# Kernel tuning notes

Measured on AMD Instinct MI355X. Metric: run time of the kernel, lower is better.

## Reference

```python
import jax, jax.numpy as jnp
import numpy as np
import math

B, SQ, SK, H, NH = 8, 512, 512, 768, 12
DH = H // NH

def setup_inputs() -> dict:
    key = jax.random.key(0)
    ks = jax.random.split(key, 8)
    s = 1.0 / math.sqrt(H)
    return {
        "hidden_states": jax.random.normal(ks[0], (B, SQ, H), jnp.float32),
        "context": jax.random.normal(ks[1], (B, SK, H), jnp.float32),
        "attention_mask": jax.random.randint(ks[2], (B, SK), 0, 2, jnp.int32),
        "Wq": jax.random.normal(ks[3], (H, H), jnp.float32) * s,
        "bq": jnp.zeros((H,), jnp.float32),
        "Wk": jax.random.normal(ks[4], (H, H), jnp.float32) * s,
        "bk": jnp.zeros((H,), jnp.float32),
        "Wv": jax.random.normal(ks[5], (H, H), jnp.float32) * s,
        "bv": jnp.zeros((H,), jnp.float32),
        "abs_pos_emb": jax.random.normal(ks[6], (512, DH), jnp.float32),
    }

def _heads(x):
    # [B, S, H] -> [B, NH, S, DH]
    b, s, _ = x.shape
    return x.reshape(b, s, NH, DH).transpose(0, 2, 1, 3)

def reference(hidden_states, context, attention_mask, Wq, bq, Wk, bk, Wv, bv, abs_pos_emb):
    q = _heads(hidden_states @ Wq.T + bq)   # [B,NH,SQ,DH]
    k = _heads(context @ Wk.T + bk)         # [B,NH,SK,DH]
    v = _heads(context @ Wv.T + bv)         # [B,NH,SK,DH]
    scores = jnp.einsum('bhqd,bhkd->bhqk', q, k)
    pos_k = abs_pos_emb[:context.shape[1]]          # [SK, DH]
    pos_q = abs_pos_emb[:hidden_states.shape[1]]    # [SQ, DH]
    pos_scores = jnp.einsum('bhqd,kd->bhqk', q + pos_q[None, None], pos_k)
    scores = (scores + pos_scores) / jnp.sqrt(jnp.float32(DH))
    mask_bias = jnp.where(attention_mask[:, None, None, :] == 0,
                          -jnp.inf, 0.0).astype(scores.dtype)
    scores = scores + mask_bias
    probs = jax.nn.softmax(scores, axis=-1)  # dropout is identity in eval
    out = jnp.einsum('bhqk,bhkd->bhqd', probs, v)
    b, _, sq, _ = out.shape
    return out.transpose(0, 2, 1, 3).reshape(b, sq, NH * DH)
```

## Files before the change

kernel.cpp:

```cpp
#include <hip/hip_runtime.h>
#include <stdint.h>

#define B_   8
#define SQ_  512
#define SK_  512
#define H_   768
#define NH_  12
#define DH_  64
#define BH_  (B_*NH_)
#define M_   (B_*SQ_)
#define NTOT (3*H_)

typedef __attribute__((ext_vector_type(8))) short short8;
typedef __attribute__((ext_vector_type(4))) float floatx4;
typedef __attribute__((ext_vector_type(4))) unsigned int uint4v;
typedef __attribute__((ext_vector_type(4))) unsigned short ushort4v;

#define MFMA16(a, b, c) __builtin_amdgcn_mfma_f32_16x16x32_bf16((a), (b), (c), 0, 0, 0)

__device__ __forceinline__ unsigned short f2b(float f) {
  union { float f; unsigned u; } c; c.f = f;
  unsigned r = (c.u + 0x7fffu + ((c.u >> 16) & 1u)) >> 16;
  return (unsigned short)r;
}
__device__ __forceinline__ float b2f(unsigned short u) {
  union { float f; unsigned u; } c; c.u = ((unsigned)u) << 16;
  return c.f;
}
__device__ __forceinline__ short8 ld8(const unsigned short* p) {
  union { uint4v u; short8 s; } c;
  c.u = *(const uint4v*)p;
  return c.s;
}

#define SEG_X   (M_*H_)
#define SEG_XC  (2*SEG_X)
#define SEG_W1  (H_*H_)
#define SEG_WE  (SEG_XC + 3*SEG_W1)
#define SEG_BE  (SEG_WE + NTOT)
#define SEG_PE  (SEG_BE + SQ_*DH_)

__global__ __launch_bounds__(256) void pack_kernel(
    const float* __restrict__ hid, const float* __restrict__ ctx,
    const float* __restrict__ Wq, const float* __restrict__ Wk, const float* __restrict__ Wv,
    const float* __restrict__ bq, const float* __restrict__ bk, const float* __restrict__ bv,
    const float* __restrict__ pos,
    unsigned short* __restrict__ Xh, unsigned short* __restrict__ Xc,
    unsigned short* __restrict__ Wa, float* __restrict__ Ba,
    unsigned short* __restrict__ Pb)
{
  int i = (blockIdx.x * 256 + threadIdx.x) * 4;
  if (i < SEG_X) {
    floatx4 v = *(const floatx4*)(hid + i);
    ushort4v o = { f2b(v.x), f2b(v.y), f2b(v.z), f2b(v.w) };
    *(ushort4v*)(Xh + i) = o;
  } else if (i < SEG_XC) {
    int j = i - SEG_X;
    floatx4 v = *(const floatx4*)(ctx + j);
    ushort4v o = { f2b(v.x), f2b(v.y), f2b(v.z), f2b(v.w) };
    *(ushort4v*)(Xc + j) = o;
  } else if (i < SEG_WE) {
    int j = i - SEG_XC;
    const float* src; int o;
    if (j < SEG_W1)        { src = Wq; o = j; }
    else if (j < 2*SEG_W1) { src = Wk; o = j - SEG_W1; }
    else                   { src = Wv; o = j - 2*SEG_W1; }
    floatx4 v = *(const floatx4*)(src + o);
    ushort4v ov = { f2b(v.x), f2b(v.y), f2b(v.z), f2b(v.w) };
    *(ushort4v*)(Wa + j) = ov;
  } else if (i < SEG_BE) {
    int j = i - SEG_WE;
    #pragma unroll
    for (int t = 0; t < 4; ++t) {
      int jj = j + t;
      float v = (jj < H_) ? bq[jj] : (jj < 2*H_) ? bk[jj - H_] : bv[jj - 2*H_];
      Ba[jj] = v;
    }
  } else if (i < SEG_PE) {
    int j = i - SEG_BE;
    floatx4 v = *(const floatx4*)(pos + j);
    ushort4v o = { f2b(v.x), f2b(v.y), f2b(v.z), f2b(v.w) };
    *(ushort4v*)(Pb + j) = o;
  }
}

__global__ __launch_bounds__(256) void qkv_gemm(
    const unsigned short* __restrict__ Xh, const unsigned short* __restrict__ Xc,
    const unsigned short* __restrict__ W,  const float* __restrict__ bias,
    const unsigned short* __restrict__ Pb,
    unsigned short* __restrict__ qw, unsigned short* __restrict__ kw,
    unsigned short* __restrict__ vt)
{
  __shared__ unsigned short As[128][72];
  __shared__ unsigned short Bs[128][72];

  int bx = blockIdx.x;
  int xcd = bx & 7, j = bx >> 3;
  int bm = (xcd >> 1) * 8 + j / 9;
  int bn = (xcd & 1) * 9 + j % 9;
  const unsigned short* X = (bn < 6) ? Xh : Xc;
  bool isV = (bn >= 12);
  int m0 = bm * 128, n0 = bn * 128;

  int tid = threadIdx.x;
  int lane = tid & 63, wave = tid >> 6;
  int wm = (wave & 1) * 64, wn = (wave >> 1) * 64;
  int lc16 = lane & 15, quad = lane >> 4, kk = quad * 8;
  int srow = tid >> 3, sch = (tid & 7) * 8;

  unsigned short (*TA)[72] = isV ? As : Bs;
  unsigned short (*TB)[72] = isV ? Bs : As;
  int oa = isV ? wm : wn;
  int ob = isV ? wn : wm;

  floatx4 acc[4][4];
  #pragma unroll
  for (int i = 0; i < 4; ++i)
    #pragma unroll
    for (int jj = 0; jj < 4; ++jj) acc[i][jj] = (floatx4){0.f, 0.f, 0.f, 0.f};

  uint4v a[4], b[4];
  #pragma unroll
  for (int rp = 0; rp < 4; ++rp) {
    a[rp] = *(const uint4v*)&X[(m0 + srow + rp * 32) * H_ + sch];
    b[rp] = *(const uint4v*)&W[(n0 + srow + rp * 32) * H_ + sch];
  }

  for (int k0 = 0; k0 < H_; k0 += 64) {
    __syncthreads();
    #pragma unroll
    for (int rp = 0; rp < 4; ++rp) {
      *(uint4v*)&As[srow + rp * 32][sch] = a[rp];
      *(uint4v*)&Bs[srow + rp * 32][sch] = b[rp];
    }
    __syncthreads();

    if (k0 + 64 < H_) {
      #pragma unroll
      for (int rp = 0; rp < 4; ++rp) {
        a[rp] = *(const uint4v*)&X[(m0 + srow + rp * 32) * H_ + k0 + 64 + sch];
        b[rp] = *(const uint4v*)&W[(n0 + srow + rp * 32) * H_ + k0 + 64 + sch];
      }
    }

    #pragma unroll
    for (int s = 0; s < 2; ++s) {
      short8 af[4], bf[4];
      #pragma unroll
      for (int i = 0; i < 4; ++i) af[i] = ld8(&TA[oa + i * 16 + lc16][s * 32 + kk]);
      #pragma unroll
      for (int i = 0; i < 4; ++i) bf[i] = ld8(&TB[ob + i * 16 + lc16][s * 32 + kk]);
      #pragma unroll
      for (int mi = 0; mi < 4; ++mi)
        #pragma unroll
        for (int ni = 0; ni < 4; ++ni)
          acc[mi][ni] = MFMA16(af[mi], bf[ni], acc[mi][ni]);
    }
  }

  if (!isV) {
    #pragma unroll
    for (int mi = 0; mi < 4; ++mi) {
      #pragma unroll
      for (int ni = 0; ni < 4; ++ni) {
        int gn0 = n0 + wn + mi * 16 + quad * 4;
        int gs  = m0 + wm + ni * 16 + lc16;
        int bidx = gs >> 9, s0 = gs & 511;
        floatx4 bv4 = *(const floatx4*)&bias[gn0];
        ushort4v o;
        if (gn0 < H_) {
          int h = gn0 >> 6, d0 = gn0 & 63;
          #pragma unroll
          for (int r = 0; r < 4; ++r) o[r] = f2b(acc[mi][ni][r] + bv4[r]);
          *(ushort4v*)(qw + (((bidx * NH_ + h) << 9) + s0) * DH_ + d0) = o;
        } else {
          int g = gn0 - H_;
          int h = g >> 6, d0 = g & 63;
          ushort4v pk = *(const ushort4v*)(Pb + s0 * DH_ + d0);
          #pragma unroll
          for (int r = 0; r < 4; ++r) o[r] = f2b(acc[mi][ni][r] + bv4[r] + b2f(pk[r]));
          *(ushort4v*)(kw + (((bidx * NH_ + h) << 9) + s0) * DH_ + d0) = o;
        }
      }
    }
  } else {
    #pragma unroll
    for (int mi = 0; mi < 4; ++mi) {
      #pragma unroll
      for (int ni = 0; ni < 4; ++ni) {
        int gm0 = m0 + wm + mi * 16 + quad * 4;
        int gn  = n0 + wn + ni * 16 + lc16;
        float bv = bias[gn];
        int bidx = gm0 >> 9, s0 = gm0 & 511;
        int g = gn - 2 * H_;
        int h = g >> 6, d = g & 63;
        ushort4v pk;
        #pragma unroll
        for (int r = 0; r < 4; ++r) pk[r] = f2b(acc[mi][ni][r] + bv);
        *(ushort4v*)(vt + ((bidx * NH_ + h) * DH_ + d) * SK_ + s0) = pk;
      }
    }
  }
}

#define SCALE2 0.18033688011112042f
#define CPAD 136

__global__ __launch_bounds__(256) void attn_kernel(
    const unsigned short* __restrict__ qw, const unsigned short* __restrict__ kw,
    const unsigned short* __restrict__ vt, const unsigned short* __restrict__ posb,
    const int* __restrict__ mask, float* __restrict__ out)
{
  __shared__ unsigned short Sc[2][64][CPAD];
  __shared__ float mb2[SK_];
  __shared__ float red[64][4];

  int bx = blockIdx.x;
  int bh = bx % 96, qt = bx / 96;
  int b = bh / NH_, h = bh - b * NH_;
  int tid = threadIdx.x, lane = tid & 63, wave = tid >> 6;
  int lc16 = lane & 15, quad = lane >> 4, kk = quad * 8;

  for (int i = tid; i < SK_; i += 256)
    mb2[i] = mask[(b << 9) + i] ? 0.0f : -100000.0f;

  const unsigned short* qbase = qw + ((bh << 9) + qt * 64) * DH_;
  const unsigned short* pqb   = posb + (qt * 64) * DH_;
  short8 aq[4][2], ap[4][2];
  #pragma unroll
  for (int rt = 0; rt < 4; ++rt) {
    const unsigned short* qr = qbase + (rt * 16 + lc16) * DH_;
    const unsigned short* pr = pqb + (rt * 16 + lc16) * DH_;
    aq[rt][0] = ld8(qr + kk);
    aq[rt][1] = ld8(qr + 32 + kk);
    ap[rt][0] = ld8(pr + kk);
    ap[rt][1] = ld8(pr + 32 + kk);
  }

  const unsigned short* kwb = kw + ((bh << 9)) * DH_;
  const unsigned short* vb0 = vt + (bh * DH_ + wave * 16 + lc16) * SK_;
  float rs[4] = {0.f, 0.f, 0.f, 0.f};
  floatx4 o[4];
  #pragma unroll
  for (int i = 0; i < 4; ++i) o[i] = (floatx4){0.f, 0.f, 0.f, 0.f};

  short8 cb0, cb1, cp0, cp1, nb0, nb1, np0, np1;
  {
    int kcol = wave * 32;
    const unsigned short* kb = kwb + kcol * DH_;
    const unsigned short* pb = posb + kcol * DH_;
    cb0 = ld8(kb + lc16 * DH_ + kk);
    cb1 = ld8(kb + lc16 * DH_ + 32 + kk);
    cp0 = ld8(pb + lc16 * DH_ + kk);
    cp1 = ld8(pb + lc16 * DH_ + 32 + kk);
  }

  __syncthreads();

  for (int chunk = 0; chunk < 4; ++chunk) {
    unsigned short (*S)[CPAD] = Sc[chunk & 1];

    short8 vf[4];
    #pragma unroll
    for (int ks = 0; ks < 4; ++ks) vf[ks] = ld8(vb0 + chunk * 128 + ks * 32 + kk);

    #pragma unroll
    for (int ct = 0; ct < 2; ++ct) {
      int s = chunk * 2 + ct;
      if (s < 7) {
        int kcol = ((s + 1) >> 1) * 128 + wave * 32 + ((s + 1) & 1) * 16;
        const unsigned short* kb = kwb + kcol * DH_;
        const unsigned short* pb = posb + kcol * DH_;
        nb0 = ld8(kb + lc16 * DH_ + kk);
        nb1 = ld8(kb + lc16 * DH_ + 32 + kk);
        np0 = ld8(pb + lc16 * DH_ + kk);
        np1 = ld8(pb + lc16 * DH_ + 32 + kk);
      }
      int kcol = chunk * 128 + wave * 32 + ct * 16;
      floatx4 mk = *(const floatx4*)&mb2[kcol + quad * 4];
      floatx4 c[4];
      #pragma unroll
      for (int rt = 0; rt < 4; ++rt) {
        c[rt] = (floatx4){0.f, 0.f, 0.f, 0.f};
        c[rt] = MFMA16(cb0, aq[rt][0], c[rt]);
        c[rt] = MFMA16(cb1, aq[rt][1], c[rt]);
        c[rt] = MFMA16(cp0, ap[rt][0], c[rt]);
        c[rt] = MFMA16(cp1, ap[rt][1], c[rt]);
      }
      int lcol = wave * 32 + ct * 16 + quad * 4;
      #pragma unroll
      for (int rt = 0; rt < 4; ++rt) {
        ushort4v pv;
        float sum = 0.f;
        #pragma unroll
        for (int r = 0; r < 4; ++r) {
          float e = __builtin_exp2f(c[rt][r] * SCALE2 + mk[r]);
          sum += e;
          pv[r] = f2b(e);
        }
        rs[rt] += sum;
        *(ushort4v*)&S[rt * 16 + lc16][lcol] = pv;
      }
      cb0 = nb0; cb1 = nb1; cp0 = np0; cp1 = np1;
    }
    __syncthreads();

    #pragma unroll
    for (int ks = 0; ks < 4; ++ks) {
      #pragma unroll
      for (int rt = 0; rt < 4; ++rt) {
        short8 pa = ld8(&S[rt * 16 + lc16][ks * 32 + kk]);
        o[rt] = MFMA16(pa, vf[ks], o[rt]);
      }
    }
  }

  #pragma unroll
  for (int rt = 0; rt < 4; ++rt) {
    rs[rt] += __shfl_xor(rs[rt], 16, 64);
    rs[rt] += __shfl_xor(rs[rt], 32, 64);
  }
  if (quad == 0) {
    #pragma unroll
    for (int rt = 0; rt < 4; ++rt) red[rt * 16 + lc16][wave] = rs[rt];
  }
  __syncthreads();

  #pragma unroll
  for (int rt = 0; rt < 4; ++rt) {
    #pragma unroll
    for (int r = 0; r < 4; ++r) {
      int sl = rt * 16 + quad * 4 + r;
      float inv = 1.0f / (red[sl][0] + red[sl][1] + red[sl][2] + red[sl][3]);
      int s = qt * 64 + sl;
      out[((b << 9) + s) * H_ + h * DH_ + wave * 16 + lc16] = o[rt][r] * inv;
    }
  }
}

extern "C" void kernel_launch(void* const* d_in, const int* in_sizes, int n_in,
                              void* d_out, int out_size, void* d_ws, size_t ws_size,
                              hipStream_t stream) {
  (void)in_sizes; (void)n_in; (void)out_size; (void)ws_size;
  const float* hid  = (const float*)d_in[0];
  const float* ctx  = (const float*)d_in[1];
  const int*   mask = (const int*)d_in[2];
  const float* Wq   = (const float*)d_in[3];
  const float* bq   = (const float*)d_in[4];
  const float* Wk   = (const float*)d_in[5];
  const float* bk   = (const float*)d_in[6];
  const float* Wv   = (const float*)d_in[7];
  const float* bv   = (const float*)d_in[8];
  const float* pos  = (const float*)d_in[9];

  char* ws = (char*)d_ws;
  size_t off = 0;
  auto alloc = [&](size_t bytes) { char* p = ws + off; off = (off + bytes + 255) & ~(size_t)255; return p; };
  unsigned short* Xh = (unsigned short*)alloc((size_t)SEG_X * 2);
  unsigned short* Xc = (unsigned short*)alloc((size_t)SEG_X * 2);
  unsigned short* Wa = (unsigned short*)alloc((size_t)3 * SEG_W1 * 2);
  float*          Ba = (float*)alloc((size_t)NTOT * 4);
  unsigned short* qw = (unsigned short*)alloc((size_t)BH_ * SQ_ * DH_ * 2);
  unsigned short* kw = (unsigned short*)alloc((size_t)BH_ * SK_ * DH_ * 2);
  unsigned short* vt = (unsigned short*)alloc((size_t)BH_ * DH_ * SK_ * 2);
  unsigned short* Pb = (unsigned short*)alloc((size_t)SQ_ * DH_ * 2);

  int pack_blocks = (SEG_PE / 4 + 255) / 256;
  pack_kernel<<<pack_blocks, 256, 0, stream>>>(hid, ctx, Wq, Wk, Wv, bq, bk, bv, pos, Xh, Xc, Wa, Ba, Pb);
  qkv_gemm<<<32 * 18, 256, 0, stream>>>(Xh, Xc, Wa, Ba, Pb, qw, kw, vt);
  attn_kernel<<<BH_ * 8, 256, 0, stream>>>(qw, kw, vt, Pb, mask, (float*)d_out);
}
```

Measured before the change: 155.4 us.

## Fuse pack, QKV GEMM and attention into one persistent kernel with grid barriers

Merges the three kernel launches into a single 768-block kernel that uses atomic-counter grid barriers between the pack, GEMM and attention phases, with shared memory unioned across phases. This removes launch overhead and the inter-kernel gaps. In exchange it depends on all 768 blocks being co-resident (launch bounds of 3 blocks per CU), leaves 192 blocks idle during the GEMM phase, and adds spin-barrier cost plus a memset launch. If the blocks cannot all be resident at once, the barrier can deadlock.

```diff
diff --git a/kernel.cpp b/kernel.cpp
--- a/kernel.cpp
+++ b/kernel.cpp
@@ -10,6 +10,7 @@
 #define BH_  (B_*NH_)
 #define M_   (B_*SQ_)
 #define NTOT (3*H_)
+#define GRID_ 768
 
 typedef __attribute__((ext_vector_type(8))) short short8;
 typedef __attribute__((ext_vector_type(4))) float floatx4;
@@ -31,6 +32,18 @@
   union { uint4v u; short8 s; } c;
   c.u = *(const uint4v*)p;
   return c.s;
+}
+
+__device__ __forceinline__ void gsync(unsigned* c) {
+  __syncthreads();
+  if (threadIdx.x == 0) {
+    __threadfence();
+    __hip_atomic_fetch_add(c, 1u, __ATOMIC_RELEASE, __HIP_MEMORY_SCOPE_AGENT);
+    while (__hip_atomic_load(c, __ATOMIC_ACQUIRE, __HIP_MEMORY_SCOPE_AGENT) < GRID_)
+      __builtin_amdgcn_s_sleep(2);
+  }
+  __syncthreads();
+  __threadfence();
 }
 
 #define SEG_X   (M_*H_)
@@ -40,300 +53,303 @@
 #define SEG_BE  (SEG_WE + NTOT)
 #define SEG_PE  (SEG_BE + SQ_*DH_)
 
-__global__ __launch_bounds__(256) void pack_kernel(
+#define SCALE2 0.18033688011112042f
+#define CPAD 136
+
+struct __align__(16) SMemG { unsigned short As[128][72]; unsigned short Bs[128][72]; };
+struct __align__(16) SMemA {
+  unsigned short Sc[2][64][CPAD];
+  float mb2[SK_];
+  float red[64][4];
+};
+union SMemU { SMemG g; SMemA a; };
+
+__global__ __launch_bounds__(256, 3) void mega_kernel(
     const float* __restrict__ hid, const float* __restrict__ ctx,
-    const float* __restrict__ Wq, const float* __restrict__ Wk, const float* __restrict__ Wv,
-    const float* __restrict__ bq, const float* __restrict__ bk, const float* __restrict__ bv,
+    const int* __restrict__ mask,
+    const float* __restrict__ Wq, const float* __restrict__ bq,
+    const float* __restrict__ Wk, const float* __restrict__ bk,
+    const float* __restrict__ Wv, const float* __restrict__ bv,
     const float* __restrict__ pos,
     unsigned short* __restrict__ Xh, unsigned short* __restrict__ Xc,
     unsigned short* __restrict__ Wa, float* __restrict__ Ba,
-    unsigned short* __restrict__ Pb)
+    unsigned short* __restrict__ Pb,
+    unsigned short* __restrict__ qw, unsigned short* __restrict__ kw,
+    unsigned short* __restrict__ vt,
+    unsigned* __restrict__ bar, float* __restrict__ out)
 {
-  int i = (blockIdx.x * 256 + threadIdx.x) * 4;
-  if (i < SEG_X) {
-    floatx4 v = *(const floatx4*)(hid + i);
-    ushort4v o = { f2b(v.x), f2b(v.y), f2b(v.z), f2b(v.w) };
-    *(ushort4v*)(Xh + i) = o;
-  } else if (i < SEG_XC) {
-    int j = i - SEG_X;
-    floatx4 v = *(const floatx4*)(ctx + j);
-    ushort4v o = { f2b(v.x), f2b(v.y), f2b(v.z), f2b(v.w) };
-    *(ushort4v*)(Xc + j) = o;
-  } else if (i < SEG_WE) {
-    int j = i - SEG_XC;
-    const float* src; int o;
-    if (j < SEG_W1)        { src = Wq; o = j; }
-    else if (j < 2*SEG_W1) { src = Wk; o = j - SEG_W1; }
-    else                   { src = Wv; o = j - 2*SEG_W1; }
-    floatx4 v = *(const floatx4*)(src + o);
-    ushort4v ov = { f2b(v.x), f2b(v.y), f2b(v.z), f2b(v.w) };
-    *(ushort4v*)(Wa + j) = ov;
-  } else if (i < SEG_BE) {
-    int j = i - SEG_WE;
-    #pragma unroll
-    for (int t = 0; t < 4; ++t) {
-      int jj = j + t;
-      float v = (jj < H_) ? bq[jj] : (jj < 2*H_) ? bk[jj - H_] : bv[jj - 2*H_];
-      Ba[jj] = v;
-    }
-  } else if (i < SEG_PE) {
-    int j = i - SEG_BE;
-    floatx4 v = *(const floatx4*)(pos + j);
-    ushort4v o = { f2b(v.x), f2b(v.y), f2b(v.z), f2b(v.w) };
-    *(ushort4v*)(Pb + j) = o;
+  __shared__ SMemU sm;
+  const int bx = blockIdx.x;
+  const int tid = threadIdx.x;
+
+  for (int v = bx * 256 + tid; v < SEG_PE / 4; v += GRID_ * 256) {
+    int i = v * 4;
+    if (i < SEG_X) {
+      floatx4 val = *(const floatx4*)(hid + i);
+      ushort4v o = { f2b(val.x), f2b(val.y), f2b(val.z), f2b(val.w) };
+      *(ushort4v*)(Xh + i) = o;
+    } else if (i < SEG_XC) {
+      int j = i - SEG_X;
+      floatx4 val = *(const floatx4*)(ctx + j);
+      ushort4v o = { f2b(val.x), f2b(val.y), f2b(val.z), f2b(val.w) };
+      *(ushort4v*)(Xc + j) = o;
+    } else if (i < SEG_WE) {
+      int j = i - SEG_XC;
+      const float* src; int o;
+      if (j < SEG_W1)        { src = Wq; o = j; }
+      else if (j < 2*SEG_W1) { src = Wk; o = j - SEG_W1; }
+      else                   { src = Wv; o = j - 2*SEG_W1; }
+      floatx4 val = *(const floatx4*)(src + o);
+      ushort4v ov = { f2b(val.x), f2b(val.y), f2b(val.z), f2b(val.w) };
+      *(ushort4v*)(Wa + j) = ov;
+    } else if (i < SEG_BE) {
+      int j = i - SEG_WE;
+      #pragma unroll
+      for (int t = 0; t < 4; ++t) {
+        int jj = j + t;
+        float val = (jj < H_) ? bq[jj] : (jj < 2*H_) ? bk[jj - H_] : bv[jj - 2*H_];
+        Ba[jj] = val;
+      }
+    } else {
+      int j = i - SEG_BE;
+      floatx4 val = *(const floatx4*)(pos + j);
+      ushort4v o = { f2b(val.x), f2b(val.y), f2b(val.z), f2b(val.w) };
+      *(ushort4v*)(Pb + j) = o;
+    }
   }
-}
-
-__global__ __launch_bounds__(256) void qkv_gemm(
-    const unsigned short* __restrict__ Xh, const unsigned short* __restrict__ Xc,
-    const unsigned short* __restrict__ W,  const float* __restrict__ bias,
-    const unsigned short* __restrict__ Pb,
-    unsigned short* __restrict__ qw, unsigned short* __restrict__ kw,
-    unsigned short* __restrict__ vt)
-{
-  __shared__ unsigned short As[128][72];
-  __shared__ unsigned short Bs[128][72];
-
-  int bx = blockIdx.x;
-  int xcd = bx & 7, j = bx >> 3;
-  int bm = (xcd >> 1) * 8 + j / 9;
-  int bn = (xcd & 1) * 9 + j % 9;
-  const unsigned short* X = (bn < 6) ? Xh : Xc;
-  bool isV = (bn >= 12);
-  int m0 = bm * 128, n0 = bn * 128;
-
-  int tid = threadIdx.x;
-  int lane = tid & 63, wave = tid >> 6;
-  int wm = (wave & 1) * 64, wn = (wave >> 1) * 64;
-  int lc16 = lane & 15, quad = lane >> 4, kk = quad * 8;
-  int srow = tid >> 3, sch = (tid & 7) * 8;
-
-  unsigned short (*TA)[72] = isV ? As : Bs;
-  unsigned short (*TB)[72] = isV ? Bs : As;
-  int oa = isV ? wm : wn;
-  int ob = isV ? wn : wm;
-
-  floatx4 acc[4][4];
-  #pragma unroll
-  for (int i = 0; i < 4; ++i)
-    #pragma unroll
-    for (int jj = 0; jj < 4; ++jj) acc[i][jj] = (floatx4){0.f, 0.f, 0.f, 0.f};
-
-  uint4v a[4], b[4];
-  #pragma unroll
-  for (int rp = 0; rp < 4; ++rp) {
-    a[rp] = *(const uint4v*)&X[(m0 + srow + rp * 32) * H_ + sch];
-    b[rp] = *(const uint4v*)&W[(n0 + srow + rp * 32) * H_ + sch];
+
+  gsync(bar + 0);
+
+  if (bx < 576) {
+    int xcd = bx & 7, j = bx >> 3;
+    int bm = (xcd >> 1) * 8 + j / 9;
+    int bn = (xcd & 1) * 9 + j % 9;
+    const unsigned short* X = (bn < 6) ? Xh : Xc;
+    bool isV = (bn >= 12);
+    int m0 = bm * 128, n0 = bn * 128;
+
+    int lane = tid & 63, wave = tid >> 6;
+    int wm = (wave & 1) * 64, wn = (wave >> 1) * 64;
+    int lc16 = lane & 15, quad = lane >> 4, kk = quad * 8;
+    int srow = tid >> 3, sch = (tid & 7) * 8;
+
+    unsigned short (*TA)[72] = isV ? sm.g.As : sm.g.Bs;
+    unsigned short (*TB)[72] = isV ? sm.g.Bs : sm.g.As;
+    int oa = isV ? wm : wn;
+    int ob = isV ? wn : wm;
+
+    floatx4 acc[4][4];
+    #pragma unroll
+    for (int i = 0; i < 4; ++i)
+      #pragma unroll
+      for (int jj = 0; jj < 4; ++jj) acc[i][jj] = (floatx4){0.f, 0.f, 0.f, 0.f};
+
+    uint4v a[4], b[4];
+    #pragma unroll
+    for (int rp = 0; rp < 4; ++rp) {
+      a[rp] = *(const uint4v*)&X[(m0 + srow + rp * 32) * H_ + sch];
+      b[rp] = *(const uint4v*)&Wa[(n0 + srow + rp * 32) * H_ + sch];
+    }
+
+    for (int k0 = 0; k0 < H_; k0 += 64) {
+      __syncthreads();
+      #pragma unroll
+      for (int rp = 0; rp < 4; ++rp) {
+        *(uint4v*)&sm.g.As[srow + rp * 32][sch] = a[rp];
+        *(uint4v*)&sm.g.Bs[srow + rp * 32][sch] = b[rp];
+      }
+      __syncthreads();
+
+      if (k0 + 64 < H_) {
+        #pragma unroll
+        for (int rp = 0; rp < 4; ++rp) {
+          a[rp] = *(const uint4v*)&X[(m0 + srow + rp * 32) * H_ + k0 + 64 + sch];
+          b[rp] = *(const uint4v*)&Wa[(n0 + srow + rp * 32) * H_ + k0 + 64 + sch];
+        }
+      }
+
+      #pragma unroll
+      for (int s = 0; s < 2; ++s) {
+        short8 af[4], bf[4];
+        #pragma unroll
+        for (int i = 0; i < 4; ++i) af[i] = ld8(&TA[oa + i * 16 + lc16][s * 32 + kk]);
+        #pragma unroll
+        for (int i = 0; i < 4; ++i) bf[i] = ld8(&TB[ob + i * 16 + lc16][s * 32 + kk]);
+        #pragma unroll
+        for (int mi = 0; mi < 4; ++mi)
+          #pragma unroll
+          for (int ni = 0; ni < 4; ++ni)
+            acc[mi][ni] = MFMA16(af[mi], bf[ni], acc[mi][ni]);
+      }
+    }
+
+    if (!isV) {
+      #pragma unroll
+      for (int mi = 0; mi < 4; ++mi) {
+        #pragma unroll
+        for (int ni = 0; ni < 4; ++ni) {
+          int gn0 = n0 + wn + mi * 16 + quad * 4;
+          int gs  = m0 + wm + ni * 16 + lc16;
+          int bidx = gs >> 9, s0 = gs & 511;
+          floatx4 bv4 = *(const floatx4*)&Ba[gn0];
+          ushort4v o;
+          if (gn0 < H_) {
+            int h = gn0 >> 6, d0 = gn0 & 63;
+            #pragma unroll
+            for (int r = 0; r < 4; ++r) o[r] = f2b(acc[mi][ni][r] + bv4[r]);
+            *(ushort4v*)(qw + (((bidx * NH_ + h) << 9) + s0) * DH_ + d0) = o;
+          } else {
+            int g = gn0 - H_;
+            int h = g >> 6, d0 = g & 63;
+            ushort4v pk = *(const ushort4v*)(Pb + s0 * DH_ + d0);
+            #pragma unroll
+            for (int r = 0; r < 4; ++r) o[r] = f2b(acc[mi][ni][r] + bv4[r] + b2f(pk[r]));
+            *(ushort4v*)(kw + (((bidx * NH_ + h) << 9) + s0) * DH_ + d0) = o;
+          }
+        }
+      }
+    } else {
+      #pragma unroll
+      for (int mi = 0; mi < 4; ++mi) {
+        #pragma unroll
+        for (int ni = 0; ni < 4; ++ni) {
+          int gm0 = m0 + wm + mi * 16 + quad * 4;
+          int gn  = n0 + wn + ni * 16 + lc16;
+          float bv = Ba[gn];
+          int bidx = gm0 >> 9, s0 = gm0 & 511;
+          int g = gn - 2 * H_;
+          int h = g >> 6, d = g & 63;
+          ushort4v pk;
+          #pragma unroll
+          for (int r = 0; r < 4; ++r) pk[r] = f2b(acc[mi][ni][r] + bv);
+          *(ushort4v*)(vt + ((bidx * NH_ + h) * DH_ + d) * SK_ + s0) = pk;
+        }
+      }
+    }
   }
 
-  for (int k0 = 0; k0 < H_; k0 += 64) {
+  gsync(bar + 1);
+
+  {
+    int bh = bx % 96, qt = bx / 96;
+    int b = bh / NH_, h = bh - b * NH_;
+    int lane = tid & 63, wave = tid >> 6;
+    int lc16 = lane & 15, quad = lane >> 4, kk = quad * 8;
+
+    for (int i = tid; i < SK_; i += 256)
+      sm.a.mb2[i] = mask[(b << 9) + i] ? 0.0f : -100000.0f;
+
+    const unsigned short* qbase = qw + ((bh << 9) + qt * 64) * DH_;
+    const unsigned short* pqb   = Pb + (qt * 64) * DH_;
+    short8 aq[4][2], ap[4][2];
+    #pragma unroll
+    for (int rt = 0; rt < 4; ++rt) {
+      const unsigned short* qr = qbase + (rt * 16 + lc16) * DH_;
+      const unsigned short* pr = pqb + (rt * 16 + lc16) * DH_;
+      aq[rt][0] = ld8(qr + kk);
+      aq[rt][1] = ld8(qr + 32 + kk);
+      ap[rt][0] = ld8(pr + kk);
+      ap[rt][1] = ld8(pr + 32 + kk);
+    }
+
+    const unsigned short* kwb = kw + ((bh << 9)) * DH_;
+    const unsigned short* vb0 = vt + (bh * DH_ + wave * 16 + lc16) * SK_;
+    float rs[4] = {0.f, 0.f, 0.f, 0.f};
+    floatx4 o[4];
+    #pragma unroll
+    for (int i = 0; i < 4; ++i) o[i] = (floatx4){0.f, 0.f, 0.f, 0.f};
+
+    short8 cb0, cb1, cp0, cp1, nb0, nb1, np0, np1;
+    {
+      int kcol = wave * 32;
+      const unsigned short* kb = kwb + kcol * DH_;
+      const unsigned short* pb = Pb + kcol * DH_;
+      cb0 = ld8(kb + lc16 * DH_ + kk);
+      cb1 = ld8(kb + lc16 * DH_ + 32 + kk);
+      cp0 = ld8(pb + lc16 * DH_ + kk);
+      cp1 = ld8(pb + lc16 * DH_ + 32 + kk);
+    }
+
     __syncthreads();
-    #pragma unroll
-    for (int rp = 0; rp < 4; ++rp) {
-      *(uint4v*)&As[srow + rp * 32][sch] = a[rp];
-      *(uint4v*)&Bs[srow + rp * 32][sch] = b[rp];
+
+    for (int chunk = 0; chunk < 4; ++chunk) {
+      unsigned short (*S)[CPAD] = sm.a.Sc[chunk & 1];
+
+      short8 vf[4];
+      #pragma unroll
+      for (int ks = 0; ks < 4; ++ks) vf[ks] = ld8(vb0 + chunk * 128 + ks * 32 + kk);
+
+      #pragma unroll
+      for (int ct = 0; ct < 2; ++ct) {
+        int s = chunk * 2 + ct;
+        if (s < 7) {
+          int kcol = ((s + 1) >> 1) * 128 + wave * 32 + ((s + 1) & 1) * 16;
+          const unsigned short* kb = kwb + kcol * DH_;
+          const unsigned short* pb = Pb + kcol * DH_;
+          nb0 = ld8(kb + lc16 * DH_ + kk);
+          nb1 = ld8(kb + lc16 * DH_ + 32 + kk);
+          np0 = ld8(pb + lc16 * DH_ + kk);
+          np1 = ld8(pb + lc16 * DH_ + 32 + kk);
+        }
+        int kcol = chunk * 128 + wave * 32 + ct * 16;
+        floatx4 mk = *(const floatx4*)&sm.a.mb2[kcol + quad * 4];
+        floatx4 c[4];
+        #pragma unroll
+        for (int rt = 0; rt < 4; ++rt) {
+          c[rt] = (floatx4){0.f, 0.f, 0.f, 0.f};
+          c[rt] = MFMA16(cb0, aq[rt][0], c[rt]);
+          c[rt] = MFMA16(cb1, aq[rt][1], c[rt]);
+          c[rt] = MFMA16(cp0, ap[rt][0], c[rt]);
+          c[rt] = MFMA16(cp1, ap[rt][1], c[rt]);
+        }
+        int lcol = wave * 32 + ct * 16 + quad * 4;
+        #pragma unroll
+        for (int rt = 0; rt < 4; ++rt) {
+          ushort4v pv;
+          float sum = 0.f;
+          #pragma unroll
+          for (int r = 0; r < 4; ++r) {
+            float e = __builtin_exp2f(c[rt][r] * SCALE2 + mk[r]);
+            sum += e;
+            pv[r] = f2b(e);
+          }
+          rs[rt] += sum;
+          *(ushort4v*)&S[rt * 16 + lc16][lcol] = pv;
+        }
+        cb0 = nb0; cb1 = nb1; cp0 = np0; cp1 = np1;
+      }
+      __syncthreads();
+
+      #pragma unroll
+      for (int ks = 0; ks < 4; ++ks) {
+        #pragma unroll
+        for (int rt = 0; rt < 4; ++rt) {
+          short8 pa = ld8(&S[rt * 16 + lc16][ks * 32 + kk]);
+          o[rt] = MFMA16(pa, vf[ks], o[rt]);
+        }
+      }
+    }
+
+    #pragma unroll
+    for (int rt = 0; rt < 4; ++rt) {
+      rs[rt] += __shfl_xor(rs[rt], 16, 64);
+      rs[rt] += __shfl_xor(rs[rt], 32, 64);
+    }
+    if (quad == 0) {
+      #pragma unroll
+      for (int rt = 0; rt < 4; ++rt) sm.a.red[rt * 16 + lc16][wave] = rs[rt];
     }
     __syncthreads();
 
-    if (k0 + 64 < H_) {
-      #pragma unroll
-      for (int rp = 0; rp < 4; ++rp) {
-        a[rp] = *(const uint4v*)&X[(m0 + srow + rp * 32) * H_ + k0 + 64 + sch];
-        b[rp] = *(const uint4v*)&W[(n0 + srow + rp * 32) * H_ + k0 + 64 + sch];
-      }
-    }
-
-    #pragma unroll
-    for (int s = 0; s < 2; ++s) {
-      short8 af[4], bf[4];
-      #pragma unroll
-      for (int i = 0; i < 4; ++i) af[i] = ld8(&TA[oa + i * 16 + lc16][s * 32 + kk]);
-      #pragma unroll
-      for (int i = 0; i < 4; ++i) bf[i] = ld8(&TB[ob + i * 16 + lc16][s * 32 + kk]);
-      #pragma unroll
-      for (int mi = 0; mi < 4; ++mi)
-        #pragma unroll
-        for (int ni = 0; ni < 4; ++ni)
-          acc[mi][ni] = MFMA16(af[mi], bf[ni], acc[mi][ni]);
-    }
-  }
-
-  if (!isV) {
-    #pragma unroll
-    for (int mi = 0; mi < 4; ++mi) {
-      #pragma unroll
-      for (int ni = 0; ni < 4; ++ni) {
-        int gn0 = n0 + wn + mi * 16 + quad * 4;
-        int gs  = m0 + wm + ni * 16 + lc16;
-        int bidx = gs >> 9, s0 = gs & 511;
-        floatx4 bv4 = *(const floatx4*)&bias[gn0];
-        ushort4v o;
-        if (gn0 < H_) {
-          int h = gn0 >> 6, d0 = gn0 & 63;
-          #pragma unroll
-          for (int r = 0; r < 4; ++r) o[r] = f2b(acc[mi][ni][r] + bv4[r]);
-          *(ushort4v*)(qw + (((bidx * NH_ + h) << 9) + s0) * DH_ + d0) = o;
-        } else {
-          int g = gn0 - H_;
-          int h = g >> 6, d0 = g & 63;
-          ushort4v pk = *(const ushort4v*)(Pb + s0 * DH_ + d0);
-          #pragma unroll
-          for (int r = 0; r < 4; ++r) o[r] = f2b(acc[mi][ni][r] + bv4[r] + b2f(pk[r]));
-          *(ushort4v*)(kw + (((bidx * NH_ + h) << 9) + s0) * DH_ + d0) = o;
-        }
-      }
-    }
-  } else {
-    #pragma unroll
-    for (int mi = 0; mi < 4; ++mi) {
-      #pragma unroll
-      for (int ni = 0; ni < 4; ++ni) {
-        int gm0 = m0 + wm + mi * 16 + quad * 4;
-        int gn  = n0 + wn + ni * 16 + lc16;
-        float bv = bias[gn];
-        int bidx = gm0 >> 9, s0 = gm0 & 511;
-        int g = gn - 2 * H_;
-        int h = g >> 6, d = g & 63;
-        ushort4v pk;
-        #pragma unroll
-        for (int r = 0; r < 4; ++r) pk[r] = f2b(acc[mi][ni][r] + bv);
-        *(ushort4v*)(vt + ((bidx * NH_ + h) * DH_ + d) * SK_ + s0) = pk;
-      }
-    }
-  }
-}
-
-#define SCALE2 0.18033688011112042f
-#define CPAD 136
-
-__global__ __launch_bounds__(256) void attn_kernel(
-    const unsigned short* __restrict__ qw, const unsigned short* __restrict__ kw,
-    const unsigned short* __restrict__ vt, const unsigned short* __restrict__ posb,
-    const int* __restrict__ mask, float* __restrict__ out)
-{
-  __shared__ unsigned short Sc[2][64][CPAD];
-  __shared__ float mb2[SK_];
-  __shared__ float red[64][4];
-
-  int bx = blockIdx.x;
-  int bh = bx % 96, qt = bx / 96;
-  int b = bh / NH_, h = bh - b * NH_;
-  int tid = threadIdx.x, lane = tid & 63, wave = tid >> 6;
-  int lc16 = lane & 15, quad = lane >> 4, kk = quad * 8;
-
-  for (int i = tid; i < SK_; i += 256)
-    mb2[i] = mask[(b << 9) + i] ? 0.0f : -100000.0f;
-
-  const unsigned short* qbase = qw + ((bh << 9) + qt * 64) * DH_;
-  const unsigned short* pqb   = posb + (qt * 64) * DH_;
-  short8 aq[4][2], ap[4][2];
-  #pragma unroll
-  for (int rt = 0; rt < 4; ++rt) {
-    const unsigned short* qr = qbase + (rt * 16 + lc16) * DH_;
-    const unsigned short* pr = pqb + (rt * 16 + lc16) * DH_;
-    aq[rt][0] = ld8(qr + kk);
-    aq[rt][1] = ld8(qr + 32 + kk);
-    ap[rt][0] = ld8(pr + kk);
-    ap[rt][1] = ld8(pr + 32 + kk);
-  }
-
-  const unsigned short* kwb = kw + ((bh << 9)) * DH_;
-  const unsigned short* vb0 = vt + (bh * DH_ + wave * 16 + lc16) * SK_;
-  float rs[4] = {0.f, 0.f, 0.f, 0.f};
-  floatx4 o[4];
-  #pragma unroll
-  for (int i = 0; i < 4; ++i) o[i] = (floatx4){0.f, 0.f, 0.f, 0.f};
-
-  short8 cb0, cb1, cp0, cp1, nb0, nb1, np0, np1;
-  {
-    int kcol = wave * 32;
-    const unsigned short* kb = kwb + kcol * DH_;
-    const unsigned short* pb = posb + kcol * DH_;
-    cb0 = ld8(kb + lc16 * DH_ + kk);
-    cb1 = ld8(kb + lc16 * DH_ + 32 + kk);
-    cp0 = ld8(pb + lc16 * DH_ + kk);
-    cp1 = ld8(pb + lc16 * DH_ + 32 + kk);
-  }
-
-  __syncthreads();
-
-  for (int chunk = 0; chunk < 4; ++chunk) {
-    unsigned short (*S)[CPAD] = Sc[chunk & 1];
-
-    short8 vf[4];
-    #pragma unroll
-    for (int ks = 0; ks < 4; ++ks) vf[ks] = ld8(vb0 + chunk * 128 + ks * 32 + kk);
-
-    #pragma unroll
-    for (int ct = 0; ct < 2; ++ct) {
-      int s = chunk * 2 + ct;
-      if (s < 7) {
-        int kcol = ((s + 1) >> 1) * 128 + wave * 32 + ((s + 1) & 1) * 16;
-        const unsigned short* kb = kwb + kcol * DH_;
-        const unsigned short* pb = posb + kcol * DH_;
-        nb0 = ld8(kb + lc16 * DH_ + kk);
-        nb1 = ld8(kb + lc16 * DH_ + 32 + kk);
-        np0 = ld8(pb + lc16 * DH_ + kk);
-        np1 = ld8(pb + lc16 * DH_ + 32 + kk);
-      }
-      int kcol = chunk * 128 + wave * 32 + ct * 16;
-      floatx4 mk = *(const floatx4*)&mb2[kcol + quad * 4];
-      floatx4 c[4];
-      #pragma unroll
-      for (int rt = 0; rt < 4; ++rt) {
-        c[rt] = (floatx4){0.f, 0.f, 0.f, 0.f};
-        c[rt] = MFMA16(cb0, aq[rt][0], c[rt]);
-        c[rt] = MFMA16(cb1, aq[rt][1], c[rt]);
-        c[rt] = MFMA16(cp0, ap[rt][0], c[rt]);
-        c[rt] = MFMA16(cp1, ap[rt][1], c[rt]);
-      }
-      int lcol = wave * 32 + ct * 16 + quad * 4;
-      #pragma unroll
-      for (int rt = 0; rt < 4; ++rt) {
-        ushort4v pv;
-        float sum = 0.f;
-        #pragma unroll
-        for (int r = 0; r < 4; ++r) {
-          float e = __builtin_exp2f(c[rt][r] * SCALE2 + mk[r]);
-          sum += e;
-          pv[r] = f2b(e);
-        }
-        rs[rt] += sum;
-        *(ushort4v*)&S[rt * 16 + lc16][lcol] = pv;
-      }
-      cb0 = nb0; cb1 = nb1; cp0 = np0; cp1 = np1;
-    }
-    __syncthreads();
-
-    #pragma unroll
-    for (int ks = 0; ks < 4; ++ks) {
-      #pragma unroll
-      for (int rt = 0; rt < 4; ++rt) {
-        short8 pa = ld8(&S[rt * 16 + lc16][ks * 32 + kk]);
-        o[rt] = MFMA16(pa, vf[ks], o[rt]);
-      }
-    }
-  }
-
-  #pragma unroll
-  for (int rt = 0; rt < 4; ++rt) {
-    rs[rt] += __shfl_xor(rs[rt], 16, 64);
-    rs[rt] += __shfl_xor(rs[rt], 32, 64);
-  }
-  if (quad == 0) {
-    #pragma unroll
-    for (int rt = 0; rt < 4; ++rt) red[rt * 16 + lc16][wave] = rs[rt];
-  }
-  __syncthreads();
-
-  #pragma unroll
-  for (int rt = 0; rt < 4; ++rt) {
-    #pragma unroll
-    for (int r = 0; r < 4; ++r) {
-      int sl = rt * 16 + quad * 4 + r;
-      float inv = 1.0f / (red[sl][0] + red[sl][1] + red[sl][2] + red[sl][3]);
-      int s = qt * 64 + sl;
-      out[((b << 9) + s) * H_ + h * DH_ + wave * 16 + lc16] = o[rt][r] * inv;
+    #pragma unroll
+    for (int rt = 0; rt < 4; ++rt) {
+      #pragma unroll
+      for (int r = 0; r < 4; ++r) {
+        int sl = rt * 16 + quad * 4 + r;
+        float inv = 1.0f / (sm.a.red[sl][0] + sm.a.red[sl][1] + sm.a.red[sl][2] + sm.a.red[sl][3]);
+        int s = qt * 64 + sl;
+        out[((b << 9) + s) * H_ + h * DH_ + wave * 16 + lc16] = o[rt][r] * inv;
+      }
     }
   }
 }
@@ -356,6 +372,7 @@
   char* ws = (char*)d_ws;
   size_t off = 0;
   auto alloc = [&](size_t bytes) { char* p = ws + off; off = (off + bytes + 255) & ~(size_t)255; return p; };
+  unsigned*       bar = (unsigned*)alloc(256);
   unsigned short* Xh = (unsigned short*)alloc((size_t)SEG_X * 2);
   unsigned short* Xc = (unsigned short*)alloc((size_t)SEG_X * 2);
   unsigned short* Wa = (unsigned short*)alloc((size_t)3 * SEG_W1 * 2);
@@ -365,8 +382,8 @@
   unsigned short* vt = (unsigned short*)alloc((size_t)BH_ * DH_ * SK_ * 2);
   unsigned short* Pb = (unsigned short*)alloc((size_t)SQ_ * DH_ * 2);
 
-  int pack_blocks = (SEG_PE / 4 + 255) / 256;
-  pack_kernel<<<pack_blocks, 256, 0, stream>>>(hid, ctx, Wq, Wk, Wv, bq, bk, bv, pos, Xh, Xc, Wa, Ba, Pb);
-  qkv_gemm<<<32 * 18, 256, 0, stream>>>(Xh, Xc, Wa, Ba, Pb, qw, kw, vt);
-  attn_kernel<<<BH_ * 8, 256, 0, stream>>>(qw, kw, vt, Pb, mask, (float*)d_out);
-}
+  hipMemsetAsync(bar, 0, 256, stream);
+  mega_kernel<<<GRID_, 256, 0, stream>>>(hid, ctx, mask, Wq, bq, Wk, bk, Wv, bv, pos,
+                                         Xh, Xc, Wa, Ba, Pb, qw, kw, vt,
+                                         bar, (float*)d_out);
+}
```

Measured after the change: 602.1 us. +287.4%, slower.

## Load QKV GEMM tiles straight into LDS with XOR-swizzled layout

Applied to the files above, without the earlier changes.

The QKV projection GEMM now stages its A and B tiles with global_load_lds, moving 16 bytes per lane from global memory directly into LDS. This replaces the previous path of register loads followed by LDS stores. The padded 72-column LDS arrays become dense 64-column tiles, and an XOR swizzle on 8-element chunks avoids bank conflicts on the fragment reads. The register prefetch of the next k-tile is removed, so loads are no longer overlapped with the MFMA work of the previous tile. That lost overlap may offset the cheaper staging path.

```diff
diff --git a/kernel.cpp b/kernel.cpp
--- a/kernel.cpp
+++ b/kernel.cpp
@@ -17,6 +17,11 @@
 typedef __attribute__((ext_vector_type(4))) unsigned short ushort4v;
 
 #define MFMA16(a, b, c) __builtin_amdgcn_mfma_f32_16x16x32_bf16((a), (b), (c), 0, 0, 0)
+
+typedef const __attribute__((address_space(1))) unsigned int glb_uint;
+typedef __attribute__((address_space(3))) unsigned int lds_uint;
+#define GLL(gptr, lptr) \
+  __builtin_amdgcn_global_load_lds((glb_uint*)(gptr), (lds_uint*)(lptr), 16, 0, 0)
 
 __device__ __forceinline__ unsigned short f2b(float f) {
   union { float f; unsigned u; } c; c.f = f;
@@ -91,8 +96,8 @@
     unsigned short* __restrict__ qw, unsigned short* __restrict__ kw,
     unsigned short* __restrict__ vt)
 {
-  __shared__ unsigned short As[128][72];
-  __shared__ unsigned short Bs[128][72];
+  __shared__ unsigned short As[128 * 64];
+  __shared__ unsigned short Bs[128 * 64];
 
   int bx = blockIdx.x;
   int xcd = bx & 7, j = bx >> 3;
@@ -106,10 +111,16 @@
   int lane = tid & 63, wave = tid >> 6;
   int wm = (wave & 1) * 64, wn = (wave >> 1) * 64;
   int lc16 = lane & 15, quad = lane >> 4, kk = quad * 8;
-  int srow = tid >> 3, sch = (tid & 7) * 8;
-
-  unsigned short (*TA)[72] = isV ? As : Bs;
-  unsigned short (*TB)[72] = isV ? Bs : As;
+  int sx7 = lc16 & 7;
+
+  int chl = wave * 64 + lane;
+  int sr = chl >> 3;
+  int scc = (chl & 7) ^ (sr & 7);
+  int gcol = scc * 8;
+
+  unsigned short (*TAp)[1] = nullptr; (void)TAp;
+  const unsigned short* TA = isV ? As : Bs;
+  const unsigned short* TB = isV ? Bs : As;
   int oa = isV ? wm : wn;
   int ob = isV ? wn : wm;
 
@@ -119,37 +130,28 @@
     #pragma unroll
     for (int jj = 0; jj < 4; ++jj) acc[i][jj] = (floatx4){0.f, 0.f, 0.f, 0.f};
 
-  uint4v a[4], b[4];
-  #pragma unroll
-  for (int rp = 0; rp < 4; ++rp) {
-    a[rp] = *(const uint4v*)&X[(m0 + srow + rp * 32) * H_ + sch];
-    b[rp] = *(const uint4v*)&W[(n0 + srow + rp * 32) * H_ + sch];
-  }
-
   for (int k0 = 0; k0 < H_; k0 += 64) {
     __syncthreads();
     #pragma unroll
-    for (int rp = 0; rp < 4; ++rp) {
-      *(uint4v*)&As[srow + rp * 32][sch] = a[rp];
-      *(uint4v*)&Bs[srow + rp * 32][sch] = b[rp];
+    for (int t = 0; t < 4; ++t) {
+      int r = t * 32 + sr;
+      unsigned short* la = As + (t * 256 + wave * 64) * 8;
+      unsigned short* lb = Bs + (t * 256 + wave * 64) * 8;
+      GLL(X + (m0 + r) * H_ + k0 + gcol, la);
+      GLL(W + (n0 + r) * H_ + k0 + gcol, lb);
     }
     __syncthreads();
 
-    if (k0 + 64 < H_) {
-      #pragma unroll
-      for (int rp = 0; rp < 4; ++rp) {
-        a[rp] = *(const uint4v*)&X[(m0 + srow + rp * 32) * H_ + k0 + 64 + sch];
-        b[rp] = *(const uint4v*)&W[(n0 + srow + rp * 32) * H_ + k0 + 64 + sch];
-      }
-    }
-
     #pragma unroll
     for (int s = 0; s < 2; ++s) {
+      int cs = s * 4 + quad;
       short8 af[4], bf[4];
       #pragma unroll
-      for (int i = 0; i < 4; ++i) af[i] = ld8(&TA[oa + i * 16 + lc16][s * 32 + kk]);
-      #pragma unroll
-      for (int i = 0; i < 4; ++i) bf[i] = ld8(&TB[ob + i * 16 + lc16][s * 32 + kk]);
+      for (int i = 0; i < 4; ++i)
+        af[i] = ld8(&TA[(oa + i * 16 + lc16) * 64 + ((cs ^ sx7) * 8)]);
+      #pragma unroll
+      for (int i = 0; i < 4; ++i)
+        bf[i] = ld8(&TB[(ob + i * 16 + lc16) * 64 + ((cs ^ sx7) * 8)]);
       #pragma unroll
       for (int mi = 0; mi < 4; ++mi)
         #pragma unroll
```

New measurement: 160.8 us. +3.5%, slower.
